# Optimization experiments

Hardware: AMD Instinct MI355X
Metric: run time of the kernel (lower is better)

The kernel has to match this reference:

```python
import jax, jax.numpy as jnp
import numpy as np

H, W = 64, 64
N = H * W                 # pixels
M_LOC = 2048              # unknown pixels for matting Laplacian
M_IU = 2048               # unknown pixels for intra-unknown term
NNZ_CM = 20 * N           # color-mixture nnz


def setup_inputs() -> dict:
    key = jax.random.key(0)
    k = jax.random.split(key, 15)
    inp = {}
    inp["height"] = H
    inp["width"] = W
    inp["CM_weights"] = jax.random.uniform(k[0], (N,), jnp.float32)
    inp["LOC_weights"] = jax.random.uniform(k[1], (N,), jnp.float32)
    inp["IU_weights"] = jax.random.uniform(k[2], (N,), jnp.float32)
    inp["KU_weights"] = jax.random.uniform(k[3], (N,), jnp.float32)
    inp["lmbda"] = jnp.float32(100.0)
    inp["kToUconf"] = jax.random.uniform(k[4], (N,), jnp.float32)
    inp["known"] = (jax.random.uniform(k[5], (N,)) < 0.5).astype(jnp.float32)
    inp["kToU"] = jax.random.uniform(k[6], (N,), jnp.float32)
    inp["Wcm_row"] = jax.random.randint(k[7], (NNZ_CM,), 0, N)
    inp["Wcm_col"] = jax.random.randint(k[8], (NNZ_CM,), 0, N)
    inp["Wcm_data"] = jax.random.uniform(k[9], (NNZ_CM,), jnp.float32)
    # interior pixels so all 3x3 neighbor offsets stay in [0, N)
    inp["LOC_inInd"] = jax.random.randint(k[10], (M_LOC, 1), W + 1, N - W - 1)
    inp["LOC_flows"] = jax.random.uniform(k[11], (9, 9, M_LOC), jnp.float32)
    inp["IU_inInd"] = jax.random.randint(k[12], (M_IU, 1), 0, N)
    inp["IU_flows"] = jax.random.uniform(k[13], (M_IU, 5), jnp.float32)
    inp["IU_neighInd"] = jax.random.randint(k[14], (M_IU, 5), 0, N)
    return inp


def _coo_dense(rows, cols, vals, n):
    # from_coo with duplicate (row, col) entries summed
    return jnp.zeros((n, n), vals.dtype).at[rows, cols].add(vals)


def reference(height, width, CM_weights, LOC_weights, IU_weights, KU_weights,
              lmbda, kToUconf, known, kToU, Wcm_row, Wcm_col, Wcm_data,
              LOC_inInd, LOC_flows, IU_inInd, IU_flows, IU_neighInd):
    n = height * width

    # ---- color mixture: Lcm = (diag(rowsum) - diag(cm) @ Wcm);  Lcm <- Lcm^T @ Lcm
    Wcm = _coo_dense(Wcm_row, Wcm_col, Wcm_data, n) * CM_weights[:, None]
    Lcm = jnp.diag(Wcm.sum(axis=1)) - Wcm
    Lcm = Lcm.T @ Lcm

    # ---- matting Laplacian (faithful to source: loop breaks after i == 0,
    # so only the first neighbor's rows/flows are scattered)
    w_loc = LOC_weights[LOC_inInd[:, 0]]                 # [M]
    flows = LOC_flows * w_loc[None, None, :]             # [9, 9, M]
    offs = jnp.array([-1 - width, -1, -1 + width, -width, 0, width,
                      1 - width, 1, 1 + width], dtype=LOC_inInd.dtype)
    neigh = LOC_inInd + offs[None, :]                    # [M, 9]
    m = neigh.shape[0]
    rows0 = jnp.broadcast_to(neigh[:, :1], (m, 9))       # neighInds[:, 0] tiled
    vals0 = flows[:, 0, :].T                             # [M, 9]
    Wmat = _coo_dense(rows0.reshape(-1), neigh.reshape(-1), vals0.reshape(-1), n)
    Wmat = 0.5 * (Wmat + Wmat.T)
    Lmat = jnp.diag(Wmat.sum(axis=1)) - Wmat

    # ---- intra-unknowns (5 nonlocal neighbors)
    w_iu = IU_weights[IU_inInd[:, 0]]                    # [Mi]
    f_iu = IU_flows[:, :5] * w_iu[:, None]               # [Mi, 5]
    mi = IU_inInd.shape[0]
    rows_iu = jnp.broadcast_to(IU_inInd, (mi, 5))
    Wcs = _coo_dense(rows_iu.reshape(-1), IU_neighInd[:, :5].reshape(-1),
                     f_iu.reshape(-1), n)
    Wcs = 0.5 * (Wcs + Wcs.T)
    Lcs = jnp.diag(Wcs.sum(axis=1)) - Wcs

    # ---- assemble linear system A x = b
    ku_diag = KU_weights * kToUconf
    known_diag = lmbda * known
    A = Lcs + Lmat + Lcm + jnp.diag(ku_diag + known_diag)
    b = (ku_diag + known_diag) * kToU
    return A, b
```

## Files before the change

### kernel.cpp

```cpp
#include <hip/hip_runtime.h>

#define WD 64
#define NN 4096
#define RCAP 128
#define XCAP 512

__global__ void k_scatter(const int* __restrict__ wrow, const int* __restrict__ wcol,
                          const float* __restrict__ wdata, const float* __restrict__ cmw,
                          const int* __restrict__ locInd, const float* __restrict__ locFlows,
                          const float* __restrict__ locw,
                          const int* __restrict__ iuInd, const float* __restrict__ iuFlows,
                          const int* __restrict__ iuNeigh, const float* __restrict__ iuw,
                          int nnz, int mloc, int miu,
                          int* __restrict__ curR, int* __restrict__ curC, int* __restrict__ curX,
                          float* __restrict__ rowsum,
                          int* __restrict__ scolR, float* __restrict__ svalR,
                          int* __restrict__ srowC, float* __restrict__ svalC,
                          int* __restrict__ xcol, float* __restrict__ xval) {
    int t = blockIdx.x * blockDim.x + threadIdx.x;
    if (t < nnz) {
        int r = wrow[t], c = wcol[t];
        float v = -wdata[t] * cmw[r];
        atomicAdd(&rowsum[r], wdata[t] * cmw[r]);
        int pR = atomicAdd(&curR[r], 1);
        if (pR < RCAP) { scolR[r * RCAP + pR] = c; svalR[r * RCAP + pR] = v; }
        int pC = atomicAdd(&curC[c], 1);
        if (pC < RCAP) { srowC[c * RCAP + pC] = r; svalC[c * RCAP + pC] = v; }
        return;
    }
    t -= nnz;
    if (t < mloc * 9) {
        int m = t / 9;
        int j = t - m * 9;
        const int offs[9] = {-1-WD, -1, -1+WD, -WD, 0, WD, 1-WD, 1, 1+WD};
        int ind = locInd[m];
        int r = ind - 1 - WD;
        int c = ind + offs[j];
        float h = 0.5f * locFlows[j * 9 * mloc + m] * locw[ind];
        int p1 = atomicAdd(&curX[r], 2);
        if (p1 + 1 < XCAP) {
            xcol[r * XCAP + p1] = c;     xval[r * XCAP + p1] = -h;
            xcol[r * XCAP + p1 + 1] = r; xval[r * XCAP + p1 + 1] = h;
        }
        int p2 = atomicAdd(&curX[c], 2);
        if (p2 + 1 < XCAP) {
            xcol[c * XCAP + p2] = r;     xval[c * XCAP + p2] = -h;
            xcol[c * XCAP + p2 + 1] = c; xval[c * XCAP + p2 + 1] = h;
        }
        return;
    }
    t -= mloc * 9;
    if (t < miu * 5) {
        int m = t / 5;
        int j = t - m * 5;
        int r = iuInd[m];
        int c = iuNeigh[m * 5 + j];
        float h = 0.5f * iuFlows[m * 5 + j] * iuw[r];
        int p1 = atomicAdd(&curX[r], 2);
        if (p1 + 1 < XCAP) {
            xcol[r * XCAP + p1] = c;     xval[r * XCAP + p1] = -h;
            xcol[r * XCAP + p1 + 1] = r; xval[r * XCAP + p1 + 1] = h;
        }
        int p2 = atomicAdd(&curX[c], 2);
        if (p2 + 1 < XCAP) {
            xcol[c * XCAP + p2] = r;     xval[c * XCAP + p2] = -h;
            xcol[c * XCAP + p2 + 1] = c; xval[c * XCAP + p2 + 1] = h;
        }
    }
}

__global__ void __launch_bounds__(256) k_rows(
    const int* __restrict__ curR, const int* __restrict__ scolR, const float* __restrict__ svalR,
    const int* __restrict__ curC, const int* __restrict__ srowC, const float* __restrict__ svalC,
    const int* __restrict__ curX, const int* __restrict__ xcol, const float* __restrict__ xval,
    const float* __restrict__ rowsum,
    const float* __restrict__ kuw, const float* __restrict__ conf, const float* __restrict__ known,
    const float* __restrict__ kToU, const float* __restrict__ lmbda,
    float* __restrict__ A, float* __restrict__ b) {
    __shared__ float acc[NN];
    __shared__ int   ck[RCAP + 1];
    __shared__ float cv[RCAP + 1];
    int i = blockIdx.x;
    int tid = threadIdx.x;

    float4* acc4 = (float4*)acc;
    for (int t = tid; t < NN / 4; t += 256) acc4[t] = make_float4(0.f, 0.f, 0.f, 0.f);

    int ccnt = min(curC[i], RCAP);
    int ctot = ccnt + 1;
    for (int t = tid; t < ctot; t += 256) {
        if (t < ccnt) { ck[t] = srowC[i * RCAP + t]; cv[t] = svalC[i * RCAP + t]; }
        else          { ck[t] = i;                   cv[t] = rowsum[i]; }
    }
    __syncthreads();

    int wave = tid >> 6, lane = tid & 63;
    for (int kk = wave; kk < ctot; kk += 4) {
        int k = ck[kk];
        float v = cv[kk];
        int rl = min(curR[k], RCAP);
        int rb = k * RCAP;
        for (int t = lane; t <= rl; t += 64) {
            int j; float w;
            if (t < rl) { j = scolR[rb + t]; w = svalR[rb + t]; }
            else        { j = k; w = rowsum[k]; }
            atomicAdd(&acc[j], v * w);
        }
    }
    int xc = min(curX[i], XCAP);
    for (int t = tid; t < xc; t += 256) {
        atomicAdd(&acc[xcol[i * XCAP + t]], xval[i * XCAP + t]);
    }
    if (tid == 0) {
        float d = kuw[i] * conf[i] + lmbda[0] * known[i];
        atomicAdd(&acc[i], d);
        b[i] = d * kToU[i];
    }
    __syncthreads();

    float4* out4 = (float4*)(A + (size_t)i * NN);
    for (int t = tid; t < NN / 4; t += 256) out4[t] = acc4[t];
}

extern "C" void kernel_launch(void* const* d_in, const int* in_sizes, int n_in,
                              void* d_out, int out_size, void* d_ws, size_t ws_size,
                              hipStream_t stream) {
    const float* CM_weights  = (const float*)d_in[2];
    const float* LOC_weights = (const float*)d_in[3];
    const float* IU_weights  = (const float*)d_in[4];
    const float* KU_weights  = (const float*)d_in[5];
    const float* lmbda       = (const float*)d_in[6];
    const float* kToUconf    = (const float*)d_in[7];
    const float* known       = (const float*)d_in[8];
    const float* kToU        = (const float*)d_in[9];
    const int*   Wcm_row     = (const int*)d_in[10];
    const int*   Wcm_col     = (const int*)d_in[11];
    const float* Wcm_data    = (const float*)d_in[12];
    const int*   LOC_inInd   = (const int*)d_in[13];
    const float* LOC_flows   = (const float*)d_in[14];
    const int*   IU_inInd    = (const int*)d_in[15];
    const float* IU_flows    = (const float*)d_in[16];
    const int*   IU_neighInd = (const int*)d_in[17];

    int nnz  = in_sizes[10];
    int mloc = in_sizes[13];
    int miu  = in_sizes[15];

    float* A = (float*)d_out;
    float* b = A + (size_t)NN * NN;

    int*   curR   = (int*)d_ws;
    int*   curC   = curR + NN;
    int*   curX   = curC + NN;
    float* rowsum = (float*)(curX + NN);
    int*   scolR  = (int*)(rowsum + NN);
    float* svalR  = (float*)(scolR + NN * RCAP);
    int*   srowC  = (int*)(svalR + NN * RCAP);
    float* svalC  = (float*)(srowC + NN * RCAP);
    int*   xcol   = (int*)(svalC + NN * RCAP);
    float* xval   = (float*)(xcol + NN * XCAP);

    hipMemsetAsync(curR, 0, 4 * NN * sizeof(int), stream);

    int tt = nnz + mloc * 9 + miu * 5;
    int blks = (tt + 255) / 256;
    k_scatter<<<blks, 256, 0, stream>>>(Wcm_row, Wcm_col, Wcm_data, CM_weights,
                                        LOC_inInd, LOC_flows, LOC_weights,
                                        IU_inInd, IU_flows, IU_neighInd, IU_weights,
                                        nnz, mloc, miu, curR, curC, curX, rowsum,
                                        scolR, svalR, srowC, svalC, xcol, xval);
    k_rows<<<NN, 256, 0, stream>>>(curR, scolR, svalR, curC, srowC, svalC,
                                   curX, xcol, xval, rowsum,
                                   KU_weights, kToUconf, known, kToU, lmbda, A, b);
}
```

Baseline: 142.7 us.

## Pack sparse index/value pairs as int2, split waves into half-waves, nontemporal stores

Stores each sparse entry's (column, value) pair in one int2 instead of separate index and value arrays, so each entry becomes a single 8-byte load. Per-neighbor row lengths and rowsums are prefetched into shared memory. Each 64-lane wave is split into two 32-lane halves so rows of about 20 entries waste fewer lanes. The 64 MB dense output is written with nontemporal stores to avoid polluting the cache.

```diff
diff --git a/kernel.cpp b/kernel.cpp
--- a/kernel.cpp
+++ b/kernel.cpp
@@ -4,6 +4,9 @@
 #define NN 4096
 #define RCAP 128
 #define XCAP 512
+
+typedef float v4f __attribute__((ext_vector_type(4)));
+
 
 __global__ void k_scatter(const int* __restrict__ wrow, const int* __restrict__ wcol,
                           const float* __restrict__ wdata, const float* __restrict__ cmw,
@@ -14,18 +17,17 @@
                           int nnz, int mloc, int miu,
                           int* __restrict__ curR, int* __restrict__ curC, int* __restrict__ curX,
                           float* __restrict__ rowsum,
-                          int* __restrict__ scolR, float* __restrict__ svalR,
-                          int* __restrict__ srowC, float* __restrict__ svalC,
-                          int* __restrict__ xcol, float* __restrict__ xval) {
+                          int2* __restrict__ sR, int2* __restrict__ sC, int2* __restrict__ xE) {
     int t = blockIdx.x * blockDim.x + threadIdx.x;
     if (t < nnz) {
         int r = wrow[t], c = wcol[t];
-        float v = -wdata[t] * cmw[r];
-        atomicAdd(&rowsum[r], wdata[t] * cmw[r]);
+        float pos = wdata[t] * cmw[r];
+        float v = -pos;
+        atomicAdd(&rowsum[r], pos);
         int pR = atomicAdd(&curR[r], 1);
-        if (pR < RCAP) { scolR[r * RCAP + pR] = c; svalR[r * RCAP + pR] = v; }
+        if (pR < RCAP) sR[r * RCAP + pR] = make_int2(c, __float_as_int(v));
         int pC = atomicAdd(&curC[c], 1);
-        if (pC < RCAP) { srowC[c * RCAP + pC] = r; svalC[c * RCAP + pC] = v; }
+        if (pC < RCAP) sC[c * RCAP + pC] = make_int2(r, __float_as_int(v));
         return;
     }
     t -= nnz;
@@ -39,13 +41,13 @@
         float h = 0.5f * locFlows[j * 9 * mloc + m] * locw[ind];
         int p1 = atomicAdd(&curX[r], 2);
         if (p1 + 1 < XCAP) {
-            xcol[r * XCAP + p1] = c;     xval[r * XCAP + p1] = -h;
-            xcol[r * XCAP + p1 + 1] = r; xval[r * XCAP + p1 + 1] = h;
+            xE[r * XCAP + p1]     = make_int2(c, __float_as_int(-h));
+            xE[r * XCAP + p1 + 1] = make_int2(r, __float_as_int( h));
         }
         int p2 = atomicAdd(&curX[c], 2);
         if (p2 + 1 < XCAP) {
-            xcol[c * XCAP + p2] = r;     xval[c * XCAP + p2] = -h;
-            xcol[c * XCAP + p2 + 1] = c; xval[c * XCAP + p2 + 1] = h;
+            xE[c * XCAP + p2]     = make_int2(r, __float_as_int(-h));
+            xE[c * XCAP + p2 + 1] = make_int2(c, __float_as_int( h));
         }
         return;
     }
@@ -58,21 +60,21 @@
         float h = 0.5f * iuFlows[m * 5 + j] * iuw[r];
         int p1 = atomicAdd(&curX[r], 2);
         if (p1 + 1 < XCAP) {
-            xcol[r * XCAP + p1] = c;     xval[r * XCAP + p1] = -h;
-            xcol[r * XCAP + p1 + 1] = r; xval[r * XCAP + p1 + 1] = h;
+            xE[r * XCAP + p1]     = make_int2(c, __float_as_int(-h));
+            xE[r * XCAP + p1 + 1] = make_int2(r, __float_as_int( h));
         }
         int p2 = atomicAdd(&curX[c], 2);
         if (p2 + 1 < XCAP) {
-            xcol[c * XCAP + p2] = r;     xval[c * XCAP + p2] = -h;
-            xcol[c * XCAP + p2 + 1] = c; xval[c * XCAP + p2 + 1] = h;
+            xE[c * XCAP + p2]     = make_int2(r, __float_as_int(-h));
+            xE[c * XCAP + p2 + 1] = make_int2(c, __float_as_int( h));
         }
     }
 }
 
 __global__ void __launch_bounds__(256) k_rows(
-    const int* __restrict__ curR, const int* __restrict__ scolR, const float* __restrict__ svalR,
-    const int* __restrict__ curC, const int* __restrict__ srowC, const float* __restrict__ svalC,
-    const int* __restrict__ curX, const int* __restrict__ xcol, const float* __restrict__ xval,
+    const int* __restrict__ curR, const int2* __restrict__ sR,
+    const int* __restrict__ curC, const int2* __restrict__ sC,
+    const int* __restrict__ curX, const int2* __restrict__ xE,
     const float* __restrict__ rowsum,
     const float* __restrict__ kuw, const float* __restrict__ conf, const float* __restrict__ known,
     const float* __restrict__ kToU, const float* __restrict__ lmbda,
@@ -80,36 +82,45 @@
     __shared__ float acc[NN];
     __shared__ int   ck[RCAP + 1];
     __shared__ float cv[RCAP + 1];
+    __shared__ int   crl[RCAP + 1];
+    __shared__ float crs[RCAP + 1];
     int i = blockIdx.x;
     int tid = threadIdx.x;
 
-    float4* acc4 = (float4*)acc;
-    for (int t = tid; t < NN / 4; t += 256) acc4[t] = make_float4(0.f, 0.f, 0.f, 0.f);
+    v4f* acc4 = (v4f*)acc;
+    for (int t = tid; t < NN / 4; t += 256) acc4[t] = (v4f){0.f, 0.f, 0.f, 0.f};
 
     int ccnt = min(curC[i], RCAP);
     int ctot = ccnt + 1;
     for (int t = tid; t < ctot; t += 256) {
-        if (t < ccnt) { ck[t] = srowC[i * RCAP + t]; cv[t] = svalC[i * RCAP + t]; }
-        else          { ck[t] = i;                   cv[t] = rowsum[i]; }
+        int k; float v;
+        if (t < ccnt) { int2 e = sC[i * RCAP + t]; k = e.x; v = __int_as_float(e.y); }
+        else          { k = i;                     v = rowsum[i]; }
+        ck[t] = k; cv[t] = v;
+        crl[t] = min(curR[k], RCAP);
+        crs[t] = rowsum[k];
     }
     __syncthreads();
 
     int wave = tid >> 6, lane = tid & 63;
-    for (int kk = wave; kk < ctot; kk += 4) {
+    int sub = lane >> 5, hl = lane & 31;
+    for (int kk = wave * 2 + sub; kk < ctot; kk += 8) {
         int k = ck[kk];
         float v = cv[kk];
-        int rl = min(curR[k], RCAP);
-        int rb = k * RCAP;
-        for (int t = lane; t <= rl; t += 64) {
+        int rl = crl[kk];
+        const int2* rowp = sR + k * RCAP;
+        for (int t = hl; t <= rl; t += 32) {
             int j; float w;
-            if (t < rl) { j = scolR[rb + t]; w = svalR[rb + t]; }
-            else        { j = k; w = rowsum[k]; }
+            if (t < rl) { int2 e = rowp[t]; j = e.x; w = __int_as_float(e.y); }
+            else        { j = k; w = crs[kk]; }
             atomicAdd(&acc[j], v * w);
         }
     }
     int xc = min(curX[i], XCAP);
+    const int2* xp = xE + i * XCAP;
     for (int t = tid; t < xc; t += 256) {
-        atomicAdd(&acc[xcol[i * XCAP + t]], xval[i * XCAP + t]);
+        int2 e = xp[t];
+        atomicAdd(&acc[e.x], __int_as_float(e.y));
     }
     if (tid == 0) {
         float d = kuw[i] * conf[i] + lmbda[0] * known[i];
@@ -118,8 +129,9 @@
     }
     __syncthreads();
 
-    float4* out4 = (float4*)(A + (size_t)i * NN);
-    for (int t = tid; t < NN / 4; t += 256) out4[t] = acc4[t];
+    v4f* out4 = (v4f*)(A + (size_t)i * NN);
+    for (int t = tid; t < NN / 4; t += 256)
+        __builtin_nontemporal_store(acc4[t], &out4[t]);
 }
 
 extern "C" void kernel_launch(void* const* d_in, const int* in_sizes, int n_in,
@@ -153,14 +165,11 @@
     int*   curC   = curR + NN;
     int*   curX   = curC + NN;
     float* rowsum = (float*)(curX + NN);
-    int*   scolR  = (int*)(rowsum + NN);
-    float* svalR  = (float*)(scolR + NN * RCAP);
-    int*   srowC  = (int*)(svalR + NN * RCAP);
-    float* svalC  = (float*)(srowC + NN * RCAP);
-    int*   xcol   = (int*)(svalC + NN * RCAP);
-    float* xval   = (float*)(xcol + NN * XCAP);
+    int2*  sR     = (int2*)(rowsum + NN);
+    int2*  sC     = sR + (size_t)NN * RCAP;
+    int2*  xE     = sC + (size_t)NN * RCAP;
 
-    hipMemsetAsync(curR, 0, 4 * NN * sizeof(int), stream);
+    (void)hipMemsetAsync(curR, 0, 4 * NN * sizeof(int), stream);
 
     int tt = nnz + mloc * 9 + miu * 5;
     int blks = (tt + 255) / 256;
@@ -168,8 +177,7 @@
                                         LOC_inInd, LOC_flows, LOC_weights,
                                         IU_inInd, IU_flows, IU_neighInd, IU_weights,
                                         nnz, mloc, miu, curR, curC, curX, rowsum,
-                                        scolR, svalR, srowC, svalC, xcol, xval);
-    k_rows<<<NN, 256, 0, stream>>>(curR, scolR, svalR, curC, srowC, svalC,
-                                   curX, xcol, xval, rowsum,
+                                        sR, sC, xE);
+    k_rows<<<NN, 256, 0, stream>>>(curR, sR, curC, sC, curX, xE, rowsum,
                                    KU_weights, kToUconf, known, kToU, lmbda, A, b);
 }
```

Measured after the change: 138.0 us. 3.3% less time.
